# Kernel tuning notes

Measured on AMD Instinct MI355X. Metric: run time of the kernel, lower is better.

## Reference

```python
import jax, jax.numpy as jnp
import numpy as np

B, T, C = 1, 2048, 1024
H, HKV, DH, WIN = 16, 4, 64, 128
EPS = 1e-5


def rotate_half(x):
    x1, x2 = jnp.split(x, 2, axis=-1)
    return jnp.concatenate((-x2, x1), axis=-1)


def setup_inputs() -> dict:
    key = jax.random.key(0)
    ks = jax.random.split(key, 8)
    s = 0.02
    return {
        "x": jax.random.normal(ks[0], (B, T, C), dtype=jnp.float32),
        "Wq": jax.random.normal(ks[1], (C, H * DH), dtype=jnp.float32) * s,
        "Wk": jax.random.normal(ks[2], (C, HKV * DH), dtype=jnp.float32) * s,
        "Wv": jax.random.normal(ks[3], (C, HKV * DH), dtype=jnp.float32) * s,
        "Wc": jax.random.normal(ks[4], (C, C), dtype=jnp.float32) * s,
        "Wg": jax.random.normal(ks[5], (C, H), dtype=jnp.float32) * s,
        "bg": jax.random.normal(ks[6], (H,), dtype=jnp.float32) * s,
        "rms_w": jnp.ones((C,), dtype=jnp.float32),
    }


def reference(x, Wq, Wk, Wv, Wc, Wg, bg, rms_w):
    n_rep = H // HKV
    # projections -> [B, heads, T, DH]
    q = (x @ Wq).reshape(B, T, H, DH).transpose(0, 2, 1, 3)
    k = (x @ Wk).reshape(B, T, HKV, DH).transpose(0, 2, 1, 3)
    v = (x @ Wv).reshape(B, T, HKV, DH).transpose(0, 2, 1, 3)
    # rotary embedding (freqs duplicated across the two halves)
    inv_freq = 1.0 / (10000.0 ** (jnp.arange(0, DH, 2, dtype=jnp.float32) / DH))
    freqs = jnp.arange(T, dtype=jnp.float32)[:, None] * inv_freq[None, :]
    emb = jnp.concatenate((freqs, freqs), axis=-1)  # [T, DH]
    cos, sin = jnp.cos(emb)[None, None], jnp.sin(emb)[None, None]
    q = q * cos + rotate_half(q) * sin
    k = k * cos + rotate_half(k) * sin
    # GQA: repeat kv heads (contiguous repeat matches torch expand+reshape)
    k = jnp.repeat(k, n_rep, axis=1)
    v = jnp.repeat(v, n_rep, axis=1)
    # gated decay
    gate_logits = (x @ Wg + bg).reshape(B, T, H, 1).transpose(0, 2, 1, 3)  # [B,H,T,1]
    log_alpha = jax.nn.log_sigmoid(gate_logits)
    log_in_scale = jax.nn.log_sigmoid(-gate_logits)
    k_scaled = k * jnp.exp(log_in_scale)
    la_cum = jnp.cumsum(log_alpha, axis=2)                  # [B,H,T,1]
    log_decay = la_cum - jnp.swapaxes(la_cum, 2, 3)         # [B,H,T,T]
    causal = jnp.triu(jnp.ones((T, T), dtype=bool), k=1)
    decay = jnp.exp(jnp.where(causal, -jnp.inf, log_decay))
    scores = jnp.einsum('bhtd,bhsd->bhts', q, k_scaled)
    y_global = jnp.einsum('bhts,bhsd->bhtd', scores * decay, v)
    nb = T // WIN
    qb = q.reshape(B, H, nb, WIN, DH)
    kb = k.reshape(B, H, nb, WIN, DH)
    vb = v.reshape(B, H, nb, WIN, DH)
    att = jnp.einsum('bhnqd,bhnkd->bhnqk', qb, kb) / jnp.sqrt(jnp.float32(DH))
    wmask = jnp.triu(jnp.ones((WIN, WIN), dtype=bool), k=1)
    att = jax.nn.softmax(jnp.where(wmask, -jnp.inf, att), axis=-1)
    y_local = jnp.einsum('bhnqk,bhnkd->bhnqd', att, vb).reshape(B, H, T, DH)
    # fuse, RMSNorm, output projection
    y = (y_global + y_local).transpose(0, 2, 1, 3).reshape(B, T, C)
    y = y * jax.lax.rsqrt(jnp.mean(y * y, axis=-1, keepdims=True) + EPS) * rms_w
    return y @ Wc
```

## Files before the change

### kernel.cpp

```cpp
#include <hip/hip_runtime.h>
#include <hip/hip_bf16.h>


typedef __attribute__((ext_vector_type(8))) short bf16x8;
typedef __attribute__((ext_vector_type(4))) float f32x4;

#define MFMA16(a, b, c) __builtin_amdgcn_mfma_f32_16x16x32_bf16(a, b, c, 0, 0, 0)
#define LN10000_OVER_32 0.28782313662425575f

__device__ __forceinline__ short f2b(float f) {
  __hip_bfloat16 h = __float2bfloat16(f);
  return *reinterpret_cast<short*>(&h);
}
__device__ __forceinline__ float b2f(short s) {
  return __uint_as_float(((unsigned)(unsigned short)s) << 16);
}
__device__ __forceinline__ void gload16(const void* g, void* l) {
  __builtin_amdgcn_global_load_lds(
      (const __attribute__((address_space(1))) void*)g,
      (__attribute__((address_space(3))) void*)l, 16, 0, 0);
}

__device__ __forceinline__ void transpose_cvt_body(
    const float* __restrict__ src, short* __restrict__ dst, int R, int C,
    int bx, int by, float* ts ) {
  int c0 = bx * 32, r0 = by * 32;
  int tr = threadIdx.x >> 3, tc = (threadIdx.x & 7) * 4;
  float4 v = *(const float4*)&src[(size_t)(r0 + tr) * C + c0 + tc];
  ts[tr * 33 + tc] = v.x;
  ts[tr * 33 + tc + 1] = v.y;
  ts[tr * 33 + tc + 2] = v.z;
  ts[tr * 33 + tc + 3] = v.w;
  __syncthreads();
  alignas(8) short o[4];
#pragma unroll
  for (int i = 0; i < 4; ++i) o[i] = f2b(ts[(tc + i) * 33 + tr]);
  *(uint2*)&dst[(size_t)(c0 + tr) * R + r0 + tc] = *(uint2*)o;
}

__global__ __launch_bounds__(256) void prep_fused(
    const float* __restrict__ x, const float* __restrict__ Wq,
    const float* __restrict__ Wk, const float* __restrict__ Wv,
    const float* __restrict__ Wc, const float* __restrict__ Wg,
    const float* __restrict__ bg, short* __restrict__ xb,
    short* __restrict__ wqkvT, short* __restrict__ wcT,
    float* __restrict__ g) {
  __shared__ float ts[32 * 33];
  const int j = blockIdx.x;
  const int tid = threadIdx.x;
  if (j < 2048) {
    const int t = j;
    const int h = tid & 15, chunk = tid >> 4;
    const float* xr = x + (size_t)t * 1024 + chunk * 64;
    const float* wg = Wg + (size_t)chunk * 64 * 16 + h;
    float acc = 0.f;
#pragma unroll
    for (int c = 0; c < 64; c += 4) {
      float4 xv = *(const float4*)(xr + c);
      acc = fmaf(xv.x, wg[(c + 0) * 16], acc);
      acc = fmaf(xv.y, wg[(c + 1) * 16], acc);
      acc = fmaf(xv.z, wg[(c + 2) * 16], acc);
      acc = fmaf(xv.w, wg[(c + 3) * 16], acc);
    }
    ts[chunk * 16 + h] = acc;
    __syncthreads();
    if (tid < 16) {
      float s = bg[tid];
#pragma unroll
      for (int i = 0; i < 16; ++i) s += ts[i * 16 + tid];
      g[t * 16 + tid] = s;
    }
  } else if (j < 3072) {
    int i = ((j - 2048) * 256 + tid) * 8;
    float4 a = *(const float4*)(x + i);
    float4 b = *(const float4*)(x + i + 4);
    alignas(16) short o[8] = {f2b(a.x), f2b(a.y), f2b(a.z), f2b(a.w),
                              f2b(b.x), f2b(b.y), f2b(b.z), f2b(b.w)};
    *(float4*)(xb + i) = *(float4*)o;
  } else if (j < 4096) {
    int jj = j - 3072;
    transpose_cvt_body(Wq, wqkvT, 1024, 1024, jj & 31, jj >> 5, ts);
  } else if (j < 4352) {
    int jj = j - 4096;
    transpose_cvt_body(Wk, wqkvT + 1024 * 1024, 1024, 256, jj & 7, jj >> 3, ts);
  } else if (j < 4608) {
    int jj = j - 4352;
    transpose_cvt_body(Wv, wqkvT + 1280 * 1024, 1024, 256, jj & 7, jj >> 3, ts);
  } else {
    int jj = j - 4608;
    transpose_cvt_body(Wc, wcT, 1024, 1024, jj & 31, jj >> 5, ts);
  }
}

__global__ __launch_bounds__(256) void qkv_gemm_fused(
    const short* __restrict__ A, const short* __restrict__ Bt,
    short* __restrict__ qkvb, short* __restrict__ vtb,
    short* __restrict__ ktb, const float* __restrict__ g,
    float* __restrict__ lac, float* __restrict__ insc) {
  __shared__ short As[64 * 64];
  __shared__ short Bs[64 * 64];
  __shared__ float part[256];
  const int id = blockIdx.x;
  const int tid = threadIdx.x;
  if (id >= 768) {
    const int h = id - 768;
    float vals[8];
    float local = 0.f;
#pragma unroll
    for (int i = 0; i < 8; ++i) {
      int t = tid * 8 + i;
      float gv = g[t * 16 + h];
      float la = (gv > 0.f) ? -log1pf(expf(-gv)) : (gv - log1pf(expf(gv)));
      insc[h * 2048 + t] = 1.f / (1.f + expf(gv));
      vals[i] = la;
      local += la;
    }
    part[tid] = local;
    __syncthreads();
    for (int off = 1; off < 256; off <<= 1) {
      float add = (tid >= off) ? part[tid - off] : 0.f;
      __syncthreads();
      part[tid] += add;
      __syncthreads();
    }
    float run = (tid > 0) ? part[tid - 1] : 0.f;
#pragma unroll
    for (int i = 0; i < 8; ++i) {
      run += vals[i];
      lac[h * 2048 + tid * 8 + i] = run;
    }
    return;
  }
  const int lane = tid & 63, wid = tid >> 6;
  const int l15 = lane & 15, lq = lane >> 4;
  const int jlin = id >> 3;
  const int by = (id & 7) + 8 * (jlin / 24);
  const int bx = jlin % 24;
  const int m0 = by * 64, n0 = bx * 64;
  const int K = 1024;
  const int srow = lane >> 3;
  const int sc16 = (lane & 7) ^ srow;
  f32x4 acc[4];
#pragma unroll
  for (int nt = 0; nt < 4; ++nt) acc[nt] = {0.f, 0.f, 0.f, 0.f};
  for (int kt = 0; kt < K; kt += 64) {
    __syncthreads();
#pragma unroll
    for (int i = 0; i < 2; ++i) {
      int jj = wid * 2 + i;
      int row = jj * 8 + srow;
      gload16(A + (size_t)(m0 + row) * K + kt + sc16 * 8, &As[jj * 512]);
      gload16(Bt + (size_t)(n0 + row) * K + kt + sc16 * 8, &Bs[jj * 512]);
    }
    __syncthreads();
    bf16x8 af[2], bfr[4][2];
#pragma unroll
    for (int ks = 0; ks < 2; ++ks) {
      int c16 = ks * 4 + lq;
      int ar = wid * 16 + l15;
      af[ks] = *(const bf16x8*)&As[(ar * 8 + (c16 ^ (ar & 7))) * 8];
#pragma unroll
      for (int nt = 0; nt < 4; ++nt) {
        int br = nt * 16 + l15;
        bfr[nt][ks] = *(const bf16x8*)&Bs[(br * 8 + (c16 ^ (br & 7))) * 8];
      }
    }
#pragma unroll
    for (int ks = 0; ks < 2; ++ks)
#pragma unroll
      for (int nt = 0; nt < 4; ++nt)
        acc[nt] = MFMA16(af[ks], bfr[nt][ks], acc[nt]);
  }
  const int row0 = m0 + wid * 16 + lq * 4;
  if (bx >= 20) {
#pragma unroll
    for (int nt = 0; nt < 4; ++nt) {
      int vcol = (n0 - 1280) + nt * 16 + l15;
      alignas(8) short o4[4];
#pragma unroll
      for (int r = 0; r < 4; ++r) o4[r] = f2b(acc[nt][r]);
      *(uint2*)&vtb[(size_t)vcol * 2048 + row0] = *(uint2*)o4;
    }
    return;
  }
  const bool isk = (bx >= 16);
#pragma unroll
  for (int nt = 0; nt < 2; ++nt) {
    int d = nt * 16 + l15;
    float ivf = __expf(-LN10000_OVER_32 * (float)d);
    alignas(8) short oa[4], ob[4];
#pragma unroll
    for (int r = 0; r < 4; ++r) {
      int row_g = row0 + r;
      float th = (float)row_g * ivf;
      float cs = cosf(th), sn = sinf(th);
      float a = acc[nt][r], b = acc[nt + 2][r];
      oa[r] = f2b(a * cs - b * sn);
      ob[r] = f2b(b * cs + a * sn);
      qkvb[(size_t)row_g * 1536 + n0 + d] = oa[r];
      qkvb[(size_t)row_g * 1536 + n0 + d + 32] = ob[r];
    }
    if (isk) {
      int dk = n0 - 1024 + d;
      *(uint2*)&ktb[(size_t)dk * 2048 + row0] = *(uint2*)oa;
      *(uint2*)&ktb[(size_t)(dk + 32) * 2048 + row0] = *(uint2*)ob;
    }
  }
}

__global__ __launch_bounds__(256) void p1_local(
    const short* __restrict__ qkv, const short* __restrict__ vtb,
    const short* __restrict__ ktb, const float* __restrict__ lac,
    const float* __restrict__ insc, float* __restrict__ Bmat,
    short* __restrict__ yl) {
  __shared__ short SA[64 * 64];
  __shared__ short SB[128 * 64];
  __shared__ short SC[64 * 128];
  __shared__ short SD[64 * 128];
  __shared__ float lacs[64], inss[64], gvals[64];
  const int tid = threadIdx.x, lane = tid & 63, wid = tid >> 6;
  const int l15 = lane & 15, lq = lane >> 4;
  const int h = blockIdx.y;
  const int kh = h >> 2;
  if (blockIdx.z == 0) {
    const int c = blockIdx.x;
    short* Ks = SB;
    short* Vts = SC;
    const int srow = lane >> 3;
    const int sc16 = (lane & 7) ^ srow;
#pragma unroll
    for (int i = 0; i < 2; ++i) {
      int jj = wid * 2 + i;
      int row = jj * 8 + srow;
      gload16(ktb + (size_t)(kh * 64 + row) * 2048 + c * 64 + sc16 * 8,
              &Ks[jj * 512]);
      gload16(vtb + (size_t)(kh * 64 + row) * 2048 + c * 64 + sc16 * 8,
              &Vts[jj * 512]);
    }
    if (tid < 64) {
      lacs[tid] = lac[h * 2048 + c * 64 + tid];
      inss[tid] = insc[h * 2048 + c * 64 + tid];
    }
    __syncthreads();
    if (tid < 64)
      gvals[tid] = __expf(fminf(lacs[63] - lacs[tid], 0.f)) * inss[tid];
    __syncthreads();
    const int er = wid * 16 + l15;
    bf16x8 av[2];
#pragma unroll
    for (int ks = 0; ks < 2; ++ks) {
      int c16 = ks * 4 + lq;
      bf16x8 raw = *(const bf16x8*)&Vts[(er * 8 + (c16 ^ (er & 7))) * 8];
      float4 g0 = *(const float4*)&gvals[c16 * 8];
      float4 g1 = *(const float4*)&gvals[c16 * 8 + 4];
      float gv[8] = {g0.x, g0.y, g0.z, g0.w, g1.x, g1.y, g1.z, g1.w};
      bf16x8 sc;
#pragma unroll
      for (int jx = 0; jx < 8; ++jx) sc[jx] = f2b(b2f(raw[jx]) * gv[jx]);
      av[ks] = sc;
    }
    f32x4 acc[4];
#pragma unroll
    for (int nt = 0; nt < 4; ++nt) acc[nt] = {0.f, 0.f, 0.f, 0.f};
#pragma unroll
    for (int ks = 0; ks < 2; ++ks) {
      int c16 = ks * 4 + lq;
#pragma unroll
      for (int nt = 0; nt < 4; ++nt) {
        int dr = nt * 16 + l15;
        bf16x8 bk = *(const bf16x8*)&Ks[(dr * 8 + (c16 ^ (dr & 7))) * 8];
        acc[nt] = MFMA16(av[ks], bk, acc[nt]);
      }
    }
    float* Bout = Bmat + (size_t)(h * 32 + c) * 4096;
#pragma unroll
    for (int nt = 0; nt < 4; ++nt)
#pragma unroll
      for (int r = 0; r < 4; ++r) {
        int e = wid * 16 + lq * 4 + r;
        Bout[e * 64 + nt * 16 + l15] = acc[nt][r];
      }
  } else {
    const int half = blockIdx.x & 1, wb = blockIdx.x >> 1;
    const int t0 = wb * 128;
    short* Qs = SA;
    short* Ks = SB;
    short* Vts = SC;
    short* Ps = SD;
#pragma unroll
    for (int i = 0; i < 2; ++i) {
      int cix = tid + 256 * i;
      int row = cix >> 3, cc = cix & 7;
      *(float4*)&Qs[(row * 8 + (cc ^ (row & 7))) * 8] =
          *(const float4*)&qkv[(size_t)(t0 + half * 64 + row) * 1536 + h * 64 + cc * 8];
    }
#pragma unroll
    for (int i = 0; i < 4; ++i) {
      int cix = tid + 256 * i;
      int row = cix >> 3, cc = cix & 7;
      *(float4*)&Ks[(row * 8 + (cc ^ (row & 7))) * 8] =
          *(const float4*)&qkv[(size_t)(t0 + row) * 1536 + 1024 + kh * 64 + cc * 8];
    }
#pragma unroll
    for (int i = 0; i < 4; ++i) {
      int cix = tid + 256 * i;
      int row = cix >> 4, cc = cix & 15;
      int sw = (row * 16 + ((cc & 8) | ((cc & 7) ^ (row & 7)))) * 8;
      *(float4*)&Vts[sw] =
          *(const float4*)&vtb[(size_t)(kh * 64 + row) * 2048 + t0 + cc * 8];
    }
    __syncthreads();
    const int qr = wid * 16 + l15;
    bf16x8 aq[2];
#pragma unroll
    for (int ks = 0; ks < 2; ++ks) {
      int c16 = ks * 4 + lq;
      aq[ks] = *(const bf16x8*)&Qs[(qr * 8 + (c16 ^ (qr & 7))) * 8];
    }
    f32x4 sv[2][4];
    const int nst = half + 1;
    for (int st = 0; st < nst; ++st)
#pragma unroll
      for (int nt = 0; nt < 4; ++nt) {
        int kr = st * 64 + nt * 16 + l15;
        bf16x8 bk0 = *(const bf16x8*)&Ks[(kr * 8 + ((0 + lq) ^ (kr & 7))) * 8];
        bf16x8 bk1 = *(const bf16x8*)&Ks[(kr * 8 + ((4 + lq) ^ (kr & 7))) * 8];
        f32x4 z = {0.f, 0.f, 0.f, 0.f};
        z = MFMA16(aq[0], bk0, z);
        z = MFMA16(aq[1], bk1, z);
        sv[st][nt] = z;
      }
    float mrow[4], ssum[4];
#pragma unroll
    for (int r = 0; r < 4; ++r) mrow[r] = -1e30f;
    for (int st = 0; st < nst; ++st)
#pragma unroll
      for (int nt = 0; nt < 4; ++nt) {
        int col = st * 64 + nt * 16 + l15;
#pragma unroll
        for (int r = 0; r < 4; ++r) {
          int row = half * 64 + wid * 16 + lq * 4 + r;
          float v = (col <= row) ? sv[st][nt][r] * 0.125f : -1e30f;
          sv[st][nt][r] = v;
          mrow[r] = fmaxf(mrow[r], v);
        }
      }
#pragma unroll
    for (int r = 0; r < 4; ++r) {
      for (int off = 1; off < 16; off <<= 1)
        mrow[r] = fmaxf(mrow[r], __shfl_xor(mrow[r], off, 64));
      ssum[r] = 0.f;
    }
    for (int st = 0; st < nst; ++st)
#pragma unroll
      for (int nt = 0; nt < 4; ++nt) {
        int col = st * 64 + nt * 16 + l15;
#pragma unroll
        for (int r = 0; r < 4; ++r) {
          float e = __expf(sv[st][nt][r] - mrow[r]);
          ssum[r] += e;
          int row = wid * 16 + lq * 4 + r;
          int c16 = col >> 3;
          Ps[(row * 16 + ((c16 & 8) | ((c16 & 7) ^ (row & 7)))) * 8 + (col & 7)] =
              f2b(e);
        }
      }
#pragma unroll
    for (int r = 0; r < 4; ++r) {
      for (int off = 1; off < 16; off <<= 1) ssum[r] += __shfl_xor(ssum[r], off, 64);
      ssum[r] = 1.f / ssum[r];
    }
    __syncthreads();
    f32x4 o[4];
#pragma unroll
    for (int nt = 0; nt < 4; ++nt) o[nt] = {0.f, 0.f, 0.f, 0.f};
    for (int ks = 0; ks < nst * 2; ++ks) {
      int c16 = ks * 4 + lq;
      bf16x8 ap = *(const bf16x8*)&Ps[(qr * 16 + ((c16 & 8) | ((c16 & 7) ^ (qr & 7)))) * 8];
#pragma unroll
      for (int nt = 0; nt < 4; ++nt) {
        int vr = nt * 16 + l15;
        bf16x8 bv = *(const bf16x8*)&Vts[(vr * 16 + ((c16 & 8) | ((c16 & 7) ^ (vr & 7)))) * 8];
        o[nt] = MFMA16(ap, bv, o[nt]);
      }
    }
#pragma unroll
    for (int nt = 0; nt < 4; ++nt)
#pragma unroll
      for (int r = 0; r < 4; ++r) {
        int row_g = t0 + half * 64 + wid * 16 + lq * 4 + r;
        int colg = h * 64 + nt * 16 + l15;
        yl[(size_t)row_g * 1024 + colg] = f2b(o[nt][r] * ssum[r]);
      }
  }
}

__global__ __launch_bounds__(256) void scan_kernel(
    const float* __restrict__ Bmat, const float* __restrict__ lac,
    short* __restrict__ St) {
  const int h = blockIdx.x, tid = threadIdx.x;
  __shared__ float lacE[32];
  if (tid < 32) lacE[tid] = lac[h * 2048 + tid * 64 + 63];
  __syncthreads();
  const int base = tid * 16;
  float S[16];
#pragma unroll
  for (int i = 0; i < 16; ++i) S[i] = 0.f;
  alignas(16) short z16[16];
#pragma unroll
  for (int i = 0; i < 16; ++i) z16[i] = 0;
  *(uint4*)&St[(size_t)(h * 32) * 4096 + base] = *(uint4*)z16;
  *(uint4*)&St[(size_t)(h * 32) * 4096 + base + 8] = *(uint4*)(z16 + 8);
  for (int c = 1; c < 32; ++c) {
    float a = (c >= 2) ? __expf(fminf(lacE[c - 1] - lacE[c - 2], 0.f)) : 0.f;
    const float* Bp = Bmat + (size_t)(h * 32 + c - 1) * 4096 + base;
    float4 b0 = *(const float4*)(Bp + 0);
    float4 b1 = *(const float4*)(Bp + 4);
    float4 b2 = *(const float4*)(Bp + 8);
    float4 b3 = *(const float4*)(Bp + 12);
    float bb[16] = {b0.x, b0.y, b0.z, b0.w, b1.x, b1.y, b1.z, b1.w,
                    b2.x, b2.y, b2.z, b2.w, b3.x, b3.y, b3.z, b3.w};
    alignas(16) short o16[16];
#pragma unroll
    for (int i = 0; i < 16; ++i) {
      S[i] = fmaf(a, S[i], bb[i]);
      o16[i] = f2b(S[i]);
    }
    *(uint4*)&St[(size_t)(h * 32 + c) * 4096 + base] = *(uint4*)o16;
    *(uint4*)&St[(size_t)(h * 32 + c) * 4096 + base + 8] = *(uint4*)(o16 + 8);
  }
}

__global__ __launch_bounds__(256) void global_attn_v3(
    const short* __restrict__ qkv, const short* __restrict__ vtb,
    const short* __restrict__ St, const float* __restrict__ lac,
    const float* __restrict__ insc, short* __restrict__ yg) {
  const int c = blockIdx.x, h = blockIdx.y;
  const int kh = h >> 2;
  __shared__ short Qs[64 * 64], Ks[64 * 64], Vts[64 * 64], Sts[64 * 64],
      Ps[64 * 64];
  __shared__ float lacq[64], inss[64];
  __shared__ float laprev_sh;
  const int tid = threadIdx.x, lane = tid & 63, wid = tid >> 6;
  const int l15 = lane & 15, lq = lane >> 4;
  const int srow = lane >> 3;
  const int sc16 = (lane & 7) ^ srow;
#pragma unroll
  for (int i = 0; i < 2; ++i) {
    int jj = wid * 2 + i;
    int row = jj * 8 + srow;
    gload16(qkv + (size_t)(c * 64 + row) * 1536 + h * 64 + sc16 * 8,
            &Qs[jj * 512]);
    gload16(qkv + (size_t)(c * 64 + row) * 1536 + 1024 + kh * 64 + sc16 * 8,
            &Ks[jj * 512]);
    gload16(vtb + (size_t)(kh * 64 + row) * 2048 + c * 64 + sc16 * 8,
            &Vts[jj * 512]);
    gload16(St + (size_t)(h * 32 + c) * 4096 + row * 64 + sc16 * 8,
            &Sts[jj * 512]);
  }
  if (tid < 64) {
    lacq[tid] = lac[h * 2048 + c * 64 + tid];
    inss[tid] = insc[h * 2048 + c * 64 + tid];
  }
  if (tid == 0) laprev_sh = (c > 0) ? lac[h * 2048 + c * 64 - 1] : 1e30f;
  __syncthreads();
  const int qr = wid * 16 + l15;
  bf16x8 aq[2];
#pragma unroll
  for (int ks = 0; ks < 2; ++ks) {
    int c16 = ks * 4 + lq;
    aq[ks] = *(const bf16x8*)&Qs[(qr * 8 + (c16 ^ (qr & 7))) * 8];
  }
  f32x4 sv[4];
#pragma unroll
  for (int nt = 0; nt < 4; ++nt) {
    int kr = nt * 16 + l15;
    bf16x8 bk0 = *(const bf16x8*)&Ks[(kr * 8 + ((0 + lq) ^ (kr & 7))) * 8];
    bf16x8 bk1 = *(const bf16x8*)&Ks[(kr * 8 + ((4 + lq) ^ (kr & 7))) * 8];
    f32x4 z = {0.f, 0.f, 0.f, 0.f};
    z = MFMA16(aq[0], bk0, z);
    z = MFMA16(aq[1], bk1, z);
    sv[nt] = z;
  }
#pragma unroll
  for (int nt = 0; nt < 4; ++nt) {
    int col = nt * 16 + l15;
    float ls = lacq[col], is = inss[col];
#pragma unroll
    for (int r = 0; r < 4; ++r) {
      int row = wid * 16 + lq * 4 + r;
      float d = lacq[row] - ls;
      float w = __expf(fminf(d, 0.f)) * is;
      if (col > row) w = 0.f;
      Ps[(row * 8 + ((col >> 3) ^ (row & 7))) * 8 + (col & 7)] = f2b(sv[nt][r] * w);
    }
  }
  f32x4 oi[4];
#pragma unroll
  for (int nt = 0; nt < 4; ++nt) {
    int er = nt * 16 + l15;
    bf16x8 bs0 = *(const bf16x8*)&Sts[(er * 8 + ((0 + lq) ^ (er & 7))) * 8];
    bf16x8 bs1 = *(const bf16x8*)&Sts[(er * 8 + ((4 + lq) ^ (er & 7))) * 8];
    f32x4 z = {0.f, 0.f, 0.f, 0.f};
    z = MFMA16(aq[0], bs0, z);
    z = MFMA16(aq[1], bs1, z);
    oi[nt] = z;
  }
  __syncthreads();
  bf16x8 ap[2];
#pragma unroll
  for (int ks = 0; ks < 2; ++ks) {
    int c16 = ks * 4 + lq;
    ap[ks] = *(const bf16x8*)&Ps[(qr * 8 + (c16 ^ (qr & 7))) * 8];
  }
  f32x4 o[4];
#pragma unroll
  for (int nt = 0; nt < 4; ++nt) {
    int vr = nt * 16 + l15;
    bf16x8 bv0 = *(const bf16x8*)&Vts[(vr * 8 + ((0 + lq) ^ (vr & 7))) * 8];
    bf16x8 bv1 = *(const bf16x8*)&Vts[(vr * 8 + ((4 + lq) ^ (vr & 7))) * 8];
    f32x4 z = {0.f, 0.f, 0.f, 0.f};
    z = MFMA16(ap[0], bv0, z);
    z = MFMA16(ap[1], bv1, z);
    o[nt] = z;
  }
  const float laprev = laprev_sh;
#pragma unroll
  for (int r = 0; r < 4; ++r) {
    int row = wid * 16 + lq * 4 + r;
    float rfac = __expf(fminf(lacq[row] - laprev, 0.f));
    int row_g = c * 64 + row;
#pragma unroll
    for (int nt = 0; nt < 4; ++nt) {
      int colg = h * 64 + nt * 16 + l15;
      yg[(size_t)row_g * 1024 + colg] = f2b(o[nt][r] + rfac * oi[nt][r]);
    }
  }
}

__global__ __launch_bounds__(256) void rmsnorm_fuse(
    const short* __restrict__ yg, const short* __restrict__ ylc,
    const float* __restrict__ w, short* __restrict__ yn) {
  const int t = blockIdx.x, tid = threadIdx.x;
  __shared__ float red[4];
  __shared__ float rowv[1024];
  __shared__ float scale_sh;
  float ssum = 0.f;
  for (int c = tid; c < 1024; c += 256) {
    size_t idx = (size_t)t * 1024 + c;
    float v = b2f(yg[idx]) + b2f(ylc[idx]);
    rowv[c] = v;
    ssum = fmaf(v, v, ssum);
  }
  for (int off = 32; off > 0; off >>= 1) ssum += __shfl_down(ssum, off, 64);
  const int lane = tid & 63, wd = tid >> 6;
  if (lane == 0) red[wd] = ssum;
  __syncthreads();
  if (tid == 0)
    scale_sh = rsqrtf((red[0] + red[1] + red[2] + red[3]) * (1.0f / 1024.0f) + 1e-5f);
  __syncthreads();
  const float scale = scale_sh;
  for (int c = tid; c < 1024; c += 256)
    yn[(size_t)t * 1024 + c] = f2b(rowv[c] * scale * w[c]);
}

__global__ __launch_bounds__(256) void out_gemm(
    const short* __restrict__ A, const short* __restrict__ Bt,
    float* __restrict__ C, int M, int N, int K, int nbx) {
  __shared__ short As[64 * 64];
  __shared__ short Bs[64 * 64];
  const int tid = threadIdx.x, lane = tid & 63, wid = tid >> 6;
  const int l15 = lane & 15, lq = lane >> 4;
  const int id = blockIdx.x;
  const int jlin = id >> 3;
  const int by = (id & 7) + 8 * (jlin / nbx);
  const int bx = jlin % nbx;
  const int m0 = by * 64, n0 = bx * 64;
  const int srow = lane >> 3;
  const int sc16 = (lane & 7) ^ srow;
  f32x4 acc[4];
#pragma unroll
  for (int nt = 0; nt < 4; ++nt) acc[nt] = {0.f, 0.f, 0.f, 0.f};
  for (int kt = 0; kt < K; kt += 64) {
    __syncthreads();
#pragma unroll
    for (int i = 0; i < 2; ++i) {
      int jj = wid * 2 + i;
      int row = jj * 8 + srow;
      gload16(A + (size_t)(m0 + row) * K + kt + sc16 * 8, &As[jj * 512]);
      gload16(Bt + (size_t)(n0 + row) * K + kt + sc16 * 8, &Bs[jj * 512]);
    }
    __syncthreads();
    bf16x8 af[2], bfr[4][2];
#pragma unroll
    for (int ks = 0; ks < 2; ++ks) {
      int c16 = ks * 4 + lq;
      int ar = wid * 16 + l15;
      af[ks] = *(const bf16x8*)&As[(ar * 8 + (c16 ^ (ar & 7))) * 8];
#pragma unroll
      for (int nt = 0; nt < 4; ++nt) {
        int br = nt * 16 + l15;
        bfr[nt][ks] = *(const bf16x8*)&Bs[(br * 8 + (c16 ^ (br & 7))) * 8];
      }
    }
#pragma unroll
    for (int ks = 0; ks < 2; ++ks)
#pragma unroll
      for (int nt = 0; nt < 4; ++nt)
        acc[nt] = MFMA16(af[ks], bfr[nt][ks], acc[nt]);
  }
#pragma unroll
  for (int r = 0; r < 4; ++r) {
    int row_g = m0 + wid * 16 + lq * 4 + r;
#pragma unroll
    for (int nt = 0; nt < 4; ++nt)
      C[(size_t)row_g * N + n0 + nt * 16 + l15] = acc[nt][r];
  }
}

extern "C" void kernel_launch(void* const* d_in, const int* in_sizes, int n_in,
                              void* d_out, int out_size, void* d_ws,
                              size_t ws_size, hipStream_t stream) {
  const float* x = (const float*)d_in[0];
  const float* Wq = (const float*)d_in[1];
  const float* Wk = (const float*)d_in[2];
  const float* Wv = (const float*)d_in[3];
  const float* Wc = (const float*)d_in[4];
  const float* Wg = (const float*)d_in[5];
  const float* bg = (const float*)d_in[6];
  const float* rmsw = (const float*)d_in[7];
  float* out = (float*)d_out;

  short* wqkvT = (short*)d_ws;
  short* wcT = wqkvT + 1536 * 1024;
  short* qkvb = wcT + 1024 * 1024;
  short* vtb = qkvb + 2048 * 1536;
  short* ktb = vtb + 256 * 2048;
  float* gw = (float*)(ktb + 256 * 2048);
  float* lacw = gw + 2048 * 16;
  float* inscw = lacw + 16 * 2048;
  float* Bmat = inscw + 16 * 2048;
  short* Stb = (short*)(Bmat + 16 * 32 * 4096);
  short* xb = Stb + 16 * 32 * 4096;
  short* yg = xb;
  short* ylc = xb + 2048 * 1024;
  short* yn = ylc + 2048 * 1024;

  prep_fused<<<5632, 256, 0, stream>>>(x, Wq, Wk, Wv, Wc, Wg, bg, xb, wqkvT,
                                       wcT, gw);
  qkv_gemm_fused<<<784, 256, 0, stream>>>(xb, wqkvT, qkvb, vtb, ktb, gw, lacw,
                                          inscw);
  p1_local<<<dim3(32, 16, 2), 256, 0, stream>>>(qkvb, vtb, ktb, lacw, inscw,
                                                Bmat, ylc);
  scan_kernel<<<16, 256, 0, stream>>>(Bmat, lacw, Stb);
  global_attn_v3<<<dim3(32, 16), 256, 0, stream>>>(qkvb, vtb, Stb, lacw, inscw,
                                                   yg);
  rmsnorm_fuse<<<2048, 256, 0, stream>>>(yg, ylc, rmsw, yn);
  out_gemm<<<512, 256, 0, stream>>>(yn, wcT, out, 2048, 1024, 1024, 16);
}
```

Before: 147.1 us.

## Fuse chunk-state scan into global attention and RMSNorm into output GEMM

Removes the serial scan kernel: each global-attention block now rebuilds its chunk's inter-chunk state directly from all previous chunk contributions, using decay-weighted sums read from Bmat. It also removes the standalone RMSNorm kernel. The output GEMM now adds yg and ylc, applies rms_w while staging A into LDS, accumulates per-row sums of squares, and scales the output rows at the end. This saves two launches and the round trips for St and yn, but the state rebuild grows quadratically with chunk count (later chunks read up to 31 Bmat tiles). The GEMM's A path also switches from async global-to-LDS loads to register loads plus conversion.

```diff
diff --git a/kernel.cpp b/kernel.cpp
--- a/kernel.cpp
+++ b/kernel.cpp
@@ -395,52 +395,15 @@
   }
 }
 
-__global__ __launch_bounds__(256) void scan_kernel(
-    const float* __restrict__ Bmat, const float* __restrict__ lac,
-    short* __restrict__ St) {
-  const int h = blockIdx.x, tid = threadIdx.x;
-  __shared__ float lacE[32];
-  if (tid < 32) lacE[tid] = lac[h * 2048 + tid * 64 + 63];
-  __syncthreads();
-  const int base = tid * 16;
-  float S[16];
-#pragma unroll
-  for (int i = 0; i < 16; ++i) S[i] = 0.f;
-  alignas(16) short z16[16];
-#pragma unroll
-  for (int i = 0; i < 16; ++i) z16[i] = 0;
-  *(uint4*)&St[(size_t)(h * 32) * 4096 + base] = *(uint4*)z16;
-  *(uint4*)&St[(size_t)(h * 32) * 4096 + base + 8] = *(uint4*)(z16 + 8);
-  for (int c = 1; c < 32; ++c) {
-    float a = (c >= 2) ? __expf(fminf(lacE[c - 1] - lacE[c - 2], 0.f)) : 0.f;
-    const float* Bp = Bmat + (size_t)(h * 32 + c - 1) * 4096 + base;
-    float4 b0 = *(const float4*)(Bp + 0);
-    float4 b1 = *(const float4*)(Bp + 4);
-    float4 b2 = *(const float4*)(Bp + 8);
-    float4 b3 = *(const float4*)(Bp + 12);
-    float bb[16] = {b0.x, b0.y, b0.z, b0.w, b1.x, b1.y, b1.z, b1.w,
-                    b2.x, b2.y, b2.z, b2.w, b3.x, b3.y, b3.z, b3.w};
-    alignas(16) short o16[16];
-#pragma unroll
-    for (int i = 0; i < 16; ++i) {
-      S[i] = fmaf(a, S[i], bb[i]);
-      o16[i] = f2b(S[i]);
-    }
-    *(uint4*)&St[(size_t)(h * 32 + c) * 4096 + base] = *(uint4*)o16;
-    *(uint4*)&St[(size_t)(h * 32 + c) * 4096 + base + 8] = *(uint4*)(o16 + 8);
-  }
-}
-
 __global__ __launch_bounds__(256) void global_attn_v3(
     const short* __restrict__ qkv, const short* __restrict__ vtb,
-    const short* __restrict__ St, const float* __restrict__ lac,
+    const float* __restrict__ Bmat, const float* __restrict__ lac,
     const float* __restrict__ insc, short* __restrict__ yg) {
   const int c = blockIdx.x, h = blockIdx.y;
   const int kh = h >> 2;
   __shared__ short Qs[64 * 64], Ks[64 * 64], Vts[64 * 64], Sts[64 * 64],
       Ps[64 * 64];
-  __shared__ float lacq[64], inss[64];
-  __shared__ float laprev_sh;
+  __shared__ float lacq[64], inss[64], lacE[32];
   const int tid = threadIdx.x, lane = tid & 63, wid = tid >> 6;
   const int l15 = lane & 15, lq = lane >> 4;
   const int srow = lane >> 3;
@@ -455,15 +418,44 @@
             &Ks[jj * 512]);
     gload16(vtb + (size_t)(kh * 64 + row) * 2048 + c * 64 + sc16 * 8,
             &Vts[jj * 512]);
-    gload16(St + (size_t)(h * 32 + c) * 4096 + row * 64 + sc16 * 8,
-            &Sts[jj * 512]);
   }
   if (tid < 64) {
     lacq[tid] = lac[h * 2048 + c * 64 + tid];
     inss[tid] = insc[h * 2048 + c * 64 + tid];
   }
-  if (tid == 0) laprev_sh = (c > 0) ? lac[h * 2048 + c * 64 - 1] : 1e30f;
+  if (tid >= 64 && tid < 96) lacE[tid - 64] = lac[h * 2048 + (tid - 64) * 64 + 63];
   __syncthreads();
+  const int e = tid >> 2, d0 = (tid & 3) * 16;
+  const float laE = (c > 0) ? lacE[c - 1] : 0.f;
+  float S[16];
+#pragma unroll
+  for (int i = 0; i < 16; ++i) S[i] = 0.f;
+  for (int cp = 0; cp < c; ++cp) {
+    float wgt = __expf(fminf(laE - lacE[cp], 0.f));
+    const float* Bp = Bmat + (size_t)(h * 32 + cp) * 4096 + e * 64 + d0;
+    float4 b0 = *(const float4*)(Bp + 0);
+    float4 b1 = *(const float4*)(Bp + 4);
+    float4 b2 = *(const float4*)(Bp + 8);
+    float4 b3 = *(const float4*)(Bp + 12);
+    S[0] = fmaf(wgt, b0.x, S[0]);  S[1] = fmaf(wgt, b0.y, S[1]);
+    S[2] = fmaf(wgt, b0.z, S[2]);  S[3] = fmaf(wgt, b0.w, S[3]);
+    S[4] = fmaf(wgt, b1.x, S[4]);  S[5] = fmaf(wgt, b1.y, S[5]);
+    S[6] = fmaf(wgt, b1.z, S[6]);  S[7] = fmaf(wgt, b1.w, S[7]);
+    S[8] = fmaf(wgt, b2.x, S[8]);  S[9] = fmaf(wgt, b2.y, S[9]);
+    S[10] = fmaf(wgt, b2.z, S[10]); S[11] = fmaf(wgt, b2.w, S[11]);
+    S[12] = fmaf(wgt, b3.x, S[12]); S[13] = fmaf(wgt, b3.y, S[13]);
+    S[14] = fmaf(wgt, b3.z, S[14]); S[15] = fmaf(wgt, b3.w, S[15]);
+  }
+  {
+    alignas(16) short s8[8];
+#pragma unroll
+    for (int half = 0; half < 2; ++half) {
+      int c16 = (tid & 3) * 2 + half;
+#pragma unroll
+      for (int i = 0; i < 8; ++i) s8[i] = f2b(S[half * 8 + i]);
+      *(uint4*)&Sts[(e * 8 + (c16 ^ (e & 7))) * 8] = *(uint4*)s8;
+    }
+  }
   const int qr = wid * 16 + l15;
   bf16x8 aq[2];
 #pragma unroll
@@ -495,6 +487,7 @@
       Ps[(row * 8 + ((col >> 3) ^ (row & 7))) * 8 + (col & 7)] = f2b(sv[nt][r] * w);
     }
   }
+  __syncthreads();
   f32x4 oi[4];
 #pragma unroll
   for (int nt = 0; nt < 4; ++nt) {
@@ -506,7 +499,6 @@
     z = MFMA16(aq[1], bs1, z);
     oi[nt] = z;
   }
-  __syncthreads();
   bf16x8 ap[2];
 #pragma unroll
   for (int ks = 0; ks < 2; ++ks) {
@@ -524,7 +516,7 @@
     z = MFMA16(ap[1], bv1, z);
     o[nt] = z;
   }
-  const float laprev = laprev_sh;
+  const float laprev = (c > 0) ? lacE[c - 1] : 1e30f;
 #pragma unroll
   for (int r = 0; r < 4; ++r) {
     int row = wid * 16 + lq * 4 + r;
@@ -538,57 +530,61 @@
   }
 }
 
-__global__ __launch_bounds__(256) void rmsnorm_fuse(
+__global__ __launch_bounds__(256) void out_gemm_rms(
     const short* __restrict__ yg, const short* __restrict__ ylc,
-    const float* __restrict__ w, short* __restrict__ yn) {
-  const int t = blockIdx.x, tid = threadIdx.x;
-  __shared__ float red[4];
-  __shared__ float rowv[1024];
-  __shared__ float scale_sh;
-  float ssum = 0.f;
-  for (int c = tid; c < 1024; c += 256) {
-    size_t idx = (size_t)t * 1024 + c;
-    float v = b2f(yg[idx]) + b2f(ylc[idx]);
-    rowv[c] = v;
-    ssum = fmaf(v, v, ssum);
-  }
-  for (int off = 32; off > 0; off >>= 1) ssum += __shfl_down(ssum, off, 64);
-  const int lane = tid & 63, wd = tid >> 6;
-  if (lane == 0) red[wd] = ssum;
-  __syncthreads();
-  if (tid == 0)
-    scale_sh = rsqrtf((red[0] + red[1] + red[2] + red[3]) * (1.0f / 1024.0f) + 1e-5f);
-  __syncthreads();
-  const float scale = scale_sh;
-  for (int c = tid; c < 1024; c += 256)
-    yn[(size_t)t * 1024 + c] = f2b(rowv[c] * scale * w[c]);
-}
-
-__global__ __launch_bounds__(256) void out_gemm(
-    const short* __restrict__ A, const short* __restrict__ Bt,
-    float* __restrict__ C, int M, int N, int K, int nbx) {
+    const float* __restrict__ w, const short* __restrict__ Bt,
+    float* __restrict__ C) {
   __shared__ short As[64 * 64];
   __shared__ short Bs[64 * 64];
+  __shared__ float ssq_sh[64 * 4];
+  __shared__ float sArr[64];
   const int tid = threadIdx.x, lane = tid & 63, wid = tid >> 6;
   const int l15 = lane & 15, lq = lane >> 4;
   const int id = blockIdx.x;
   const int jlin = id >> 3;
-  const int by = (id & 7) + 8 * (jlin / nbx);
-  const int bx = jlin % nbx;
+  const int by = (id & 7) + 8 * (jlin / 16);
+  const int bx = jlin % 16;
   const int m0 = by * 64, n0 = bx * 64;
   const int srow = lane >> 3;
   const int sc16 = (lane & 7) ^ srow;
+  const int arow = tid >> 2, akc = (tid & 3) * 16;
   f32x4 acc[4];
 #pragma unroll
   for (int nt = 0; nt < 4; ++nt) acc[nt] = {0.f, 0.f, 0.f, 0.f};
-  for (int kt = 0; kt < K; kt += 64) {
+  float ssq = 0.f;
+  for (int kt = 0; kt < 1024; kt += 64) {
     __syncthreads();
 #pragma unroll
     for (int i = 0; i < 2; ++i) {
       int jj = wid * 2 + i;
       int row = jj * 8 + srow;
-      gload16(A + (size_t)(m0 + row) * K + kt + sc16 * 8, &As[jj * 512]);
-      gload16(Bt + (size_t)(n0 + row) * K + kt + sc16 * 8, &Bs[jj * 512]);
+      gload16(Bt + (size_t)(n0 + row) * 1024 + kt + sc16 * 8, &Bs[jj * 512]);
+    }
+    {
+      const size_t ab = (size_t)(m0 + arow) * 1024 + kt + akc;
+      bf16x8 g0 = *(const bf16x8*)&yg[ab];
+      bf16x8 g1 = *(const bf16x8*)&yg[ab + 8];
+      bf16x8 L0 = *(const bf16x8*)&ylc[ab];
+      bf16x8 L1 = *(const bf16x8*)&ylc[ab + 8];
+      float4 w0 = *(const float4*)&w[kt + akc];
+      float4 w1 = *(const float4*)&w[kt + akc + 4];
+      float4 w2 = *(const float4*)&w[kt + akc + 8];
+      float4 w3 = *(const float4*)&w[kt + akc + 12];
+      float wv[16] = {w0.x, w0.y, w0.z, w0.w, w1.x, w1.y, w1.z, w1.w,
+                      w2.x, w2.y, w2.z, w2.w, w3.x, w3.y, w3.z, w3.w};
+      alignas(16) short p0[8], p1[8];
+#pragma unroll
+      for (int i = 0; i < 8; ++i) {
+        float yv = b2f(g0[i]) + b2f(L0[i]);
+        ssq = fmaf(yv, yv, ssq);
+        p0[i] = f2b(yv * wv[i]);
+        float yv2 = b2f(g1[i]) + b2f(L1[i]);
+        ssq = fmaf(yv2, yv2, ssq);
+        p1[i] = f2b(yv2 * wv[8 + i]);
+      }
+      int c16a = (tid & 3) * 2;
+      *(uint4*)&As[(arow * 8 + (c16a ^ (arow & 7))) * 8] = *(uint4*)p0;
+      *(uint4*)&As[(arow * 8 + ((c16a + 1) ^ (arow & 7))) * 8] = *(uint4*)p1;
     }
     __syncthreads();
     bf16x8 af[2], bfr[4][2];
@@ -609,12 +605,23 @@
       for (int nt = 0; nt < 4; ++nt)
         acc[nt] = MFMA16(af[ks], bfr[nt][ks], acc[nt]);
   }
+  __syncthreads();
+  ssq_sh[arow * 4 + (tid & 3)] = ssq;
+  __syncthreads();
+  if (tid < 64) {
+    float s = ssq_sh[tid * 4] + ssq_sh[tid * 4 + 1] + ssq_sh[tid * 4 + 2] +
+              ssq_sh[tid * 4 + 3];
+    sArr[tid] = rsqrtf(s * (1.0f / 1024.0f) + 1e-5f);
+  }
+  __syncthreads();
 #pragma unroll
   for (int r = 0; r < 4; ++r) {
-    int row_g = m0 + wid * 16 + lq * 4 + r;
+    int row = wid * 16 + lq * 4 + r;
+    float scale = sArr[row];
+    int row_g = m0 + row;
 #pragma unroll
     for (int nt = 0; nt < 4; ++nt)
-      C[(size_t)row_g * N + n0 + nt * 16 + l15] = acc[nt][r];
+      C[(size_t)row_g * 1024 + n0 + nt * 16 + l15] = acc[nt][r] * scale;
   }
 }
 
@@ -640,11 +647,9 @@
   float* lacw = gw + 2048 * 16;
   float* inscw = lacw + 16 * 2048;
   float* Bmat = inscw + 16 * 2048;
-  short* Stb = (short*)(Bmat + 16 * 32 * 4096);
-  short* xb = Stb + 16 * 32 * 4096;
+  short* xb = (short*)(Bmat + 16 * 32 * 4096);
   short* yg = xb;
   short* ylc = xb + 2048 * 1024;
-  short* yn = ylc + 2048 * 1024;
 
   prep_fused<<<5632, 256, 0, stream>>>(x, Wq, Wk, Wv, Wc, Wg, bg, xb, wqkvT,
                                        wcT, gw);
@@ -652,9 +657,7 @@
                                           inscw);
   p1_local<<<dim3(32, 16, 2), 256, 0, stream>>>(qkvb, vtb, ktb, lacw, inscw,
                                                 Bmat, ylc);
-  scan_kernel<<<16, 256, 0, stream>>>(Bmat, lacw, Stb);
-  global_attn_v3<<<dim3(32, 16), 256, 0, stream>>>(qkvb, vtb, Stb, lacw, inscw,
-                                                   yg);
-  rmsnorm_fuse<<<2048, 256, 0, stream>>>(yg, ylc, rmsw, yn);
-  out_gemm<<<512, 256, 0, stream>>>(yn, wcT, out, 2048, 1024, 1024, 16);
-}
+  global_attn_v3<<<dim3(32, 16), 256, 0, stream>>>(qkvb, vtb, Bmat, lacw,
+                                                   inscw, yg);
+  out_gemm_rms<<<512, 256, 0, stream>>>(yg, ylc, rmsw, wcT, out);
+}
```

After: 149.0 us. No clear change (+1.3%).
